# Kernel optimization log

Hardware: AMD Instinct MI355X
Metric: run time of the kernel (lower is better)

Reference implementation:

```python
import jax, jax.numpy as jnp
import numpy as np

L, S, N, E, H = 1024, 1024, 8, 1024, 16

def setup_inputs() -> dict:
    key = jax.random.key(0)
    k0, k1, k2, k3 = jax.random.split(key, 4)
    query = jax.random.normal(k0, (L, N, E), jnp.float32)
    key_t = jax.random.normal(k1, (S, N, E), jnp.float32)
    in_proj_weight = jax.random.normal(k2, (3 * E, E), jnp.float32) * (1.0 / np.sqrt(E))
    in_proj_bias = jnp.zeros((3 * E,), jnp.float32)
    attn_bias = jax.random.normal(k3, (N * H, L, S), jnp.float32) * 0.02
    return {"query": query, "key": key_t, "in_proj_weight": in_proj_weight,
            "in_proj_bias": in_proj_bias, "attn_bias": attn_bias}

def reference(query, key, in_proj_weight, in_proj_bias, attn_bias):
    tgt_len, bsz, embed_dim = query.shape
    head_dim = embed_dim // H
    scaling = float(head_dim) ** -0.5  # scale_factor = 1
    # q/k projections: first two embed_dim-row slices of in_proj_weight
    q = query @ in_proj_weight[:embed_dim].T + in_proj_bias[:embed_dim]
    k = key @ in_proj_weight[embed_dim:2 * embed_dim].T + in_proj_bias[embed_dim:2 * embed_dim]
    q = q * scaling
    # (L, N, E) -> (N*H, L, hd)
    q = q.reshape(tgt_len, bsz * H, head_dim).transpose(1, 0, 2)
    k = k.reshape(-1, bsz * H, head_dim).transpose(1, 0, 2)
    # scores: (N*H, L, S), additive bias, then stable softmax
    scores = jnp.einsum('bld,bsd->bls', q, k) + attn_bias
    attn_output_weights = jax.nn.softmax(scores, axis=-1)
    return attn_output_weights
```

## Files before the change

kernel.cpp:

```cpp
#include <hip/hip_runtime.h>
#include <hip/hip_bf16.h>
#include <stdint.h>

#define L_DIM 1024
#define S_DIM 1024
#define N_DIM 8
#define E_DIM 1024
#define H_DIM 16
#define HD    64
#define BH    (N_DIM*H_DIM)
#define M_ROWS (L_DIM*N_DIM)

#define AS1 __attribute__((address_space(1)))
#define AS3 __attribute__((address_space(3)))

typedef __bf16 bf16x8 __attribute__((ext_vector_type(8)));
typedef float  f32x4  __attribute__((ext_vector_type(4)));
typedef _Float16 f16;
typedef _Float16 f16x8 __attribute__((ext_vector_type(8)));
typedef unsigned short u16;
typedef unsigned short u16x8 __attribute__((ext_vector_type(8)));

__device__ inline u16 f2bf(float x){
  unsigned int u = __float_as_uint(x);
  u = (u + 0x7FFFu + ((u >> 16) & 1u)) >> 16;
  return (u16)u;
}

__global__ __launch_bounds__(256) void convert_kernel(
    const float* __restrict__ query, const float* __restrict__ key,
    const float* __restrict__ w,
    u16* __restrict__ qbf, u16* __restrict__ kbf,
    u16* __restrict__ wq, u16* __restrict__ wk)
{
  const int QN = M_ROWS*E_DIM;
  const int WN = E_DIM*E_DIM;
  const int total8 = (2*QN + 2*WN)/8;
  int stride = gridDim.x*blockDim.x;
  for (int g = blockIdx.x*blockDim.x + threadIdx.x; g < total8; g += stride) {
    int base = g*8;
    const float* src; u16* dst; float scale = 1.0f;
    if (base < QN)           { src = query + base;      dst = qbf + base; }
    else if (base < 2*QN)    { src = key + (base-QN);   dst = kbf + (base-QN); }
    else if (base < 2*QN+WN) { src = w + (base-2*QN);   dst = wq + (base-2*QN); scale = 0.125f; }
    else                     { src = w + (base-2*QN);   dst = wk + (base-2*QN-WN); }
    float4 v0 = *(const float4*)(src);
    float4 v1 = *(const float4*)(src+4);
    u16x8 o;
    o[0]=f2bf(v0.x*scale); o[1]=f2bf(v0.y*scale); o[2]=f2bf(v0.z*scale); o[3]=f2bf(v0.w*scale);
    o[4]=f2bf(v1.x*scale); o[5]=f2bf(v1.y*scale); o[6]=f2bf(v1.z*scale); o[7]=f2bf(v1.w*scale);
    *(u16x8*)dst = o;
  }
}

__global__ __launch_bounds__(256) void proj_gemm(
    const u16* __restrict__ A, const u16* __restrict__ W,
    const float* __restrict__ bias, float bscale,
    u16* __restrict__ C)
{
  __shared__ __align__(16) u16 As[128*32];
  __shared__ __align__(16) u16 Bs[128*32];
  const int t = threadIdx.x;
  const int lane = t & 63;
  const int w = t >> 6;
  const int wr = w >> 1, wc = w & 1;
  const int rowTile = blockIdx.x * 128;
  const int colTile = blockIdx.y * 128;

  f32x4 acc[4][4];
  #pragma unroll
  for (int m=0;m<4;m++)
    #pragma unroll
    for (int n=0;n<4;n++) acc[m][n] = (f32x4){0.f,0.f,0.f,0.f};

  uint32_t asBase = (uint32_t)(uintptr_t)&As[0];
  uint32_t bsBase = (uint32_t)(uintptr_t)&Bs[0];
  const char* Ab = (const char*)A;
  const char* Wb = (const char*)W;

  for (int kt = 0; kt < 32; ++kt) {
    __syncthreads();
    #pragma unroll
    for (int issue = 0; issue < 2; ++issue) {
      int o = issue*4096 + t*16;
      int row  = o >> 6;
      int colb = o & 63;
      const char* ga = Ab + (size_t)(rowTile + row)*2048 + kt*64 + colb;
      const char* gb = Wb + (size_t)(colTile + row)*2048 + kt*64 + colb;
      uint32_t la = asBase + issue*4096 + (w<<10);
      uint32_t lb = bsBase + issue*4096 + (w<<10);
      __builtin_amdgcn_global_load_lds(
          (const AS1 void*)(uintptr_t)ga, (AS3 void*)(uintptr_t)la, 16, 0, 0);
      __builtin_amdgcn_global_load_lds(
          (const AS1 void*)(uintptr_t)gb, (AS3 void*)(uintptr_t)lb, 16, 0, 0);
    }
    __syncthreads();

    bf16x8 af[4], bfr[4];
    int krow = (lane >> 4) * 16;
    #pragma unroll
    for (int m=0;m<4;m++) {
      int r = wr*64 + m*16 + (lane&15);
      af[m] = *(const bf16x8*)((const char*)As + r*64 + krow);
    }
    #pragma unroll
    for (int n=0;n<4;n++) {
      int r = wc*64 + n*16 + (lane&15);
      bfr[n] = *(const bf16x8*)((const char*)Bs + r*64 + krow);
    }
    #pragma unroll
    for (int m=0;m<4;m++)
      #pragma unroll
      for (int n=0;n<4;n++)
        acc[m][n] = __builtin_amdgcn_mfma_f32_16x16x32_bf16(af[m], bfr[n], acc[m][n], 0,0,0);
  }

  #pragma unroll
  for (int n2=0;n2<4;n2++) {
    int gcol = colTile + wc*64 + n2*16 + (lane&15);
    int h = gcol >> 6, d = gcol & 63;
    float bv = bias[gcol]*bscale;
    #pragma unroll
    for (int m=0;m<4;m++) {
      int grow0 = rowTile + wr*64 + m*16 + ((lane>>4)<<2);
      #pragma unroll
      for (int r=0;r<4;r++) {
        int grow = grow0 + r;
        int l = grow >> 3, nn = grow & 7;
        C[((size_t)(nn*16 + h)*1024 + l)*64 + d] = f2bf(acc[m][n2][r] + bv);
      }
    }
  }
}

__global__ __launch_bounds__(256) void attn_softmax(
    const u16* __restrict__ Qh, const u16* __restrict__ Kh,
    const float* __restrict__ bias, float* __restrict__ out)
{
  __shared__ __align__(16) char scb[16*2048];
  __shared__ __align__(16) char kbuf[8192];
  const int t = threadIdx.x;
  const int lane = t & 63;
  const int w = t >> 6;
  const int ltile = blockIdx.x;
  const int b = blockIdx.y;

  const char* Kb = (const char*)(Kh + (size_t)b*1024*64);
  const u16*  Qb = Qh + (size_t)b*1024*64 + (size_t)ltile*16*64;

  int qoff = (lane&15)*64 + (lane>>4)*8;
  bf16x8 a0 = *(const bf16x8*)(Qb + qoff);
  bf16x8 a1 = *(const bf16x8*)(Qb + qoff + 32);

  const int rowBase = (lane>>4)*4;
  uint32_t kbase = (uint32_t)(uintptr_t)&kbuf[0];

  for (int g = 0; g < 16; ++g) {
    __syncthreads();
    #pragma unroll
    for (int rd = 0; rd < 2; ++rd) {
      int o = rd*4096 + t*16;
      int src = o ^ (((o>>7)&7)<<4);
      __builtin_amdgcn_global_load_lds(
          (const AS1 void*)(uintptr_t)(Kb + (size_t)g*8192 + src),
          (AS3 void*)(uintptr_t)(kbase + rd*4096 + (w<<10)), 16, 0, 0);
    }
    __syncthreads();

    int r = w*16 + (lane&15);
    int byte0 = r*128 + ((lane>>4)*16);
    int swzk = (r&7)<<4;
    bf16x8 b0 = *(const bf16x8*)(kbuf + ((byte0      ) ^ swzk));
    bf16x8 b1 = *(const bf16x8*)(kbuf + ((byte0 + 64 ) ^ swzk));
    f32x4 acc = {0.f,0.f,0.f,0.f};
    acc = __builtin_amdgcn_mfma_f32_16x16x32_bf16(a0, b0, acc, 0,0,0);
    acc = __builtin_amdgcn_mfma_f32_16x16x32_bf16(a1, b1, acc, 0,0,0);

    int scol = g*64 + w*16 + (lane & 15);
    #pragma unroll
    for (int rr=0;rr<4;rr++) {
      int row = rowBase + rr;
      int byte = (row*2048 + scol*2) ^ ((row&7)<<4);
      *(f16*)(scb + byte) = (f16)acc[rr];
    }
  }
  __syncthreads();

  #pragma unroll
  for (int rr=0;rr<4;rr++) {
    int row = rr*4 + w;
    int l_glob = ltile*16 + row;
    const float* brow = bias + ((size_t)b*1024 + l_glob)*1024;
    float*       orow = out  + ((size_t)b*1024 + l_glob)*1024;
    const int swz = (row&7)<<4;
    float v[16];
    float mx = -1e30f;
    #pragma unroll
    for (int it=0; it<2; ++it) {
      int cb = it*1024 + lane*16;
      f16x8 s8 = *(const f16x8*)(scb + ((row*2048 + cb) ^ swz));
      int col = it*512 + lane*8;
      f32x4 b4a = *(const f32x4*)(brow + col);
      f32x4 b4b = *(const f32x4*)(brow + col + 4);
      #pragma unroll
      for (int j=0;j<4;j++) v[it*8+j]   = (float)s8[j]   + b4a[j];
      #pragma unroll
      for (int j=0;j<4;j++) v[it*8+4+j] = (float)s8[4+j] + b4b[j];
    }
    #pragma unroll
    for (int j=0;j<16;j++) mx = fmaxf(mx, v[j]);
    #pragma unroll
    for (int off=32; off>0; off>>=1) mx = fmaxf(mx, __shfl_xor(mx, off, 64));
    float sum = 0.f;
    #pragma unroll
    for (int j=0;j<16;j++) { v[j] = __expf(v[j]-mx); sum += v[j]; }
    #pragma unroll
    for (int off=32; off>0; off>>=1) sum += __shfl_xor(sum, off, 64);
    float inv = 1.0f / sum;
    #pragma unroll
    for (int it=0; it<2; ++it) {
      int col = it*512 + lane*8;
      f32x4 o4a = { v[it*8+0]*inv, v[it*8+1]*inv, v[it*8+2]*inv, v[it*8+3]*inv };
      f32x4 o4b = { v[it*8+4]*inv, v[it*8+5]*inv, v[it*8+6]*inv, v[it*8+7]*inv };
      *(f32x4*)(orow + col)     = o4a;
      *(f32x4*)(orow + col + 4) = o4b;
    }
  }
}

extern "C" void kernel_launch(void* const* d_in, const int* in_sizes, int n_in,
                              void* d_out, int out_size, void* d_ws, size_t ws_size,
                              hipStream_t stream) {
  const float* query = (const float*)d_in[0];
  const float* key   = (const float*)d_in[1];
  const float* w     = (const float*)d_in[2];
  const float* bias  = (const float*)d_in[3];
  const float* abias = (const float*)d_in[4];
  float* out = (float*)d_out;

  char* ws = (char*)d_ws;
  const size_t QKB = (size_t)M_ROWS*E_DIM*2;
  const size_t WB  = (size_t)E_DIM*E_DIM*2;
  u16* qbf = (u16*)ws;  ws += QKB;
  u16* kbf = (u16*)ws;  ws += QKB;
  u16* wq  = (u16*)ws;  ws += WB;
  u16* wk  = (u16*)ws;  ws += WB;
  u16* Qh  = (u16*)ws;  ws += QKB;
  u16* Kh  = (u16*)ws;  ws += QKB;

  hipLaunchKernelGGL(convert_kernel, dim3(2048), dim3(256), 0, stream,
                     query, key, w, qbf, kbf, wq, wk);
  hipLaunchKernelGGL(proj_gemm, dim3(64, 8), dim3(256), 0, stream,
                     qbf, wq, bias, 0.125f, Qh);
  hipLaunchKernelGGL(proj_gemm, dim3(64, 8), dim3(256), 0, stream,
                     kbf, wk, bias + 1024, 1.0f, Kh);
  hipLaunchKernelGGL(attn_softmax, dim3(64, 128), dim3(256), 0, stream,
                     Qh, Kh, abias, out);
}
```

Measured before the change: 322.3 us.

## Compute transposed scores in registers with bias-initialized accumulators, drop LDS staging

The attention-softmax kernel now computes K·Q^T with MFMA so each lane holds four consecutive score columns for one query row. The accumulators are initialized straight from the attention bias, and the fp16 LDS score buffer and the K staging through LDS are removed. Row max and sum are reduced with shuffles plus a small LDS cross-wave exchange. This removes the shared-memory round trip and the per-K-chunk barriers, and it keeps scores in fp32 instead of fp16. In exchange it uses more registers (64 accumulators per lane) and reads K directly from global memory in each wave.

After: 419.0 us. +30.0%, slower.

```diff
diff --git a/kernel.cpp b/kernel.cpp
--- a/kernel.cpp
+++ b/kernel.cpp
@@ -16,8 +16,6 @@
 
 typedef __bf16 bf16x8 __attribute__((ext_vector_type(8)));
 typedef float  f32x4  __attribute__((ext_vector_type(4)));
-typedef _Float16 f16;
-typedef _Float16 f16x8 __attribute__((ext_vector_type(8)));
 typedef unsigned short u16;
 typedef unsigned short u16x8 __attribute__((ext_vector_type(8)));
 
@@ -137,94 +135,73 @@
     const u16* __restrict__ Qh, const u16* __restrict__ Kh,
     const float* __restrict__ bias, float* __restrict__ out)
 {
-  __shared__ __align__(16) char scb[16*2048];
-  __shared__ __align__(16) char kbuf[8192];
+  __shared__ float red_max[4][16];
+  __shared__ float red_sum[4][16];
   const int t = threadIdx.x;
   const int lane = t & 63;
   const int w = t >> 6;
   const int ltile = blockIdx.x;
   const int b = blockIdx.y;
-
-  const char* Kb = (const char*)(Kh + (size_t)b*1024*64);
-  const u16*  Qb = Qh + (size_t)b*1024*64 + (size_t)ltile*16*64;
-
-  int qoff = (lane&15)*64 + (lane>>4)*8;
-  bf16x8 a0 = *(const bf16x8*)(Qb + qoff);
-  bf16x8 a1 = *(const bf16x8*)(Qb + qoff + 32);
-
-  const int rowBase = (lane>>4)*4;
-  uint32_t kbase = (uint32_t)(uintptr_t)&kbuf[0];
-
-  for (int g = 0; g < 16; ++g) {
-    __syncthreads();
-    #pragma unroll
-    for (int rd = 0; rd < 2; ++rd) {
-      int o = rd*4096 + t*16;
-      int src = o ^ (((o>>7)&7)<<4);
-      __builtin_amdgcn_global_load_lds(
-          (const AS1 void*)(uintptr_t)(Kb + (size_t)g*8192 + src),
-          (AS3 void*)(uintptr_t)(kbase + rd*4096 + (w<<10)), 16, 0, 0);
-    }
-    __syncthreads();
-
-    int r = w*16 + (lane&15);
-    int byte0 = r*128 + ((lane>>4)*16);
-    int swzk = (r&7)<<4;
-    bf16x8 b0 = *(const bf16x8*)(kbuf + ((byte0      ) ^ swzk));
-    bf16x8 b1 = *(const bf16x8*)(kbuf + ((byte0 + 64 ) ^ swzk));
-    f32x4 acc = {0.f,0.f,0.f,0.f};
-    acc = __builtin_amdgcn_mfma_f32_16x16x32_bf16(a0, b0, acc, 0,0,0);
-    acc = __builtin_amdgcn_mfma_f32_16x16x32_bf16(a1, b1, acc, 0,0,0);
-
-    int scol = g*64 + w*16 + (lane & 15);
-    #pragma unroll
-    for (int rr=0;rr<4;rr++) {
-      int row = rowBase + rr;
-      int byte = (row*2048 + scol*2) ^ ((row&7)<<4);
-      *(f16*)(scb + byte) = (f16)acc[rr];
-    }
-  }
+  const int q  = lane & 15;
+  const int sg = lane >> 4;
+
+  const u16* Qb = Qh + (size_t)b*65536 + (size_t)ltile*16*64;
+  bf16x8 a0 = *(const bf16x8*)(Qb + q*64 + sg*8);
+  bf16x8 a1 = *(const bf16x8*)(Qb + q*64 + sg*8 + 32);
+
+  const u16* Kw = Kh + (size_t)b*65536 + (size_t)w*16384 + (lane&15)*64 + sg*8;
+
+  const size_t rowoff = (((size_t)b<<10) + (size_t)ltile*16 + q)*1024 + w*256 + sg*4;
+  const float* bp = bias + rowoff;
+  float*       op = out  + rowoff;
+
+  f32x4 acc[16];
+  #pragma unroll
+  for (int st = 0; st < 16; ++st)
+    acc[st] = *(const f32x4*)(bp + st*16);
+
+  #pragma unroll
+  for (int st = 0; st < 16; ++st) {
+    const u16* kp = Kw + st*1024;
+    bf16x8 k0 = *(const bf16x8*)kp;
+    bf16x8 k1 = *(const bf16x8*)(kp + 32);
+    acc[st] = __builtin_amdgcn_mfma_f32_16x16x32_bf16(k0, a0, acc[st], 0,0,0);
+    acc[st] = __builtin_amdgcn_mfma_f32_16x16x32_bf16(k1, a1, acc[st], 0,0,0);
+  }
+
+  float mx = fmaxf(fmaxf(acc[0][0], acc[0][1]), fmaxf(acc[0][2], acc[0][3]));
+  #pragma unroll
+  for (int st = 1; st < 16; ++st) {
+    mx = fmaxf(mx, fmaxf(fmaxf(acc[st][0], acc[st][1]),
+                         fmaxf(acc[st][2], acc[st][3])));
+  }
+  mx = fmaxf(mx, __shfl_xor(mx, 16, 64));
+  mx = fmaxf(mx, __shfl_xor(mx, 32, 64));
+  if (lane < 16) red_max[w][lane] = mx;
   __syncthreads();
-
-  #pragma unroll
-  for (int rr=0;rr<4;rr++) {
-    int row = rr*4 + w;
-    int l_glob = ltile*16 + row;
-    const float* brow = bias + ((size_t)b*1024 + l_glob)*1024;
-    float*       orow = out  + ((size_t)b*1024 + l_glob)*1024;
-    const int swz = (row&7)<<4;
-    float v[16];
-    float mx = -1e30f;
-    #pragma unroll
-    for (int it=0; it<2; ++it) {
-      int cb = it*1024 + lane*16;
-      f16x8 s8 = *(const f16x8*)(scb + ((row*2048 + cb) ^ swz));
-      int col = it*512 + lane*8;
-      f32x4 b4a = *(const f32x4*)(brow + col);
-      f32x4 b4b = *(const f32x4*)(brow + col + 4);
-      #pragma unroll
-      for (int j=0;j<4;j++) v[it*8+j]   = (float)s8[j]   + b4a[j];
-      #pragma unroll
-      for (int j=0;j<4;j++) v[it*8+4+j] = (float)s8[4+j] + b4b[j];
-    }
-    #pragma unroll
-    for (int j=0;j<16;j++) mx = fmaxf(mx, v[j]);
-    #pragma unroll
-    for (int off=32; off>0; off>>=1) mx = fmaxf(mx, __shfl_xor(mx, off, 64));
-    float sum = 0.f;
-    #pragma unroll
-    for (int j=0;j<16;j++) { v[j] = __expf(v[j]-mx); sum += v[j]; }
-    #pragma unroll
-    for (int off=32; off>0; off>>=1) sum += __shfl_xor(sum, off, 64);
-    float inv = 1.0f / sum;
-    #pragma unroll
-    for (int it=0; it<2; ++it) {
-      int col = it*512 + lane*8;
-      f32x4 o4a = { v[it*8+0]*inv, v[it*8+1]*inv, v[it*8+2]*inv, v[it*8+3]*inv };
-      f32x4 o4b = { v[it*8+4]*inv, v[it*8+5]*inv, v[it*8+6]*inv, v[it*8+7]*inv };
-      *(f32x4*)(orow + col)     = o4a;
-      *(f32x4*)(orow + col + 4) = o4b;
-    }
+  mx = fmaxf(fmaxf(red_max[0][q], red_max[1][q]),
+             fmaxf(red_max[2][q], red_max[3][q]));
+
+  float sum = 0.f;
+  #pragma unroll
+  for (int st = 0; st < 16; ++st) {
+    #pragma unroll
+    for (int r = 0; r < 4; ++r) {
+      float e = __expf(acc[st][r] - mx);
+      acc[st][r] = e;
+      sum += e;
+    }
+  }
+  sum += __shfl_xor(sum, 16, 64);
+  sum += __shfl_xor(sum, 32, 64);
+  if (lane < 16) red_sum[w][lane] = sum;
+  __syncthreads();
+  float inv = 1.0f / (red_sum[0][q] + red_sum[1][q] + red_sum[2][q] + red_sum[3][q]);
+
+  #pragma unroll
+  for (int st = 0; st < 16; ++st) {
+    f32x4 o4 = { acc[st][0]*inv, acc[st][1]*inv, acc[st][2]*inv, acc[st][3]*inv };
+    *(f32x4*)(op + st*16) = o4;
   }
 }
 
```

## Fuse fp32-to-bf16 activation conversion into projection GEMM tile loads

Applied to the files above, without the earlier changes.

Removes the separate conversion pass for query and key: the projection GEMM now loads fp32 activation tiles directly into LDS with an XOR swizzle and converts to bf16 while building MFMA fragments. Only the weights are still pre-converted by a smaller kernel. This removes a large intermediate write and read round trip, at the cost of doubled A-tile LDS footprint, wider global loads per tile, and conversion work inside the inner loop.

Result: slower. 335.6 us (+4.1%).

```diff
diff --git a/kernel.cpp b/kernel.cpp
--- a/kernel.cpp
+++ b/kernel.cpp
@@ -16,6 +16,7 @@
 
 typedef __bf16 bf16x8 __attribute__((ext_vector_type(8)));
 typedef float  f32x4  __attribute__((ext_vector_type(4)));
+typedef float  f32x8  __attribute__((ext_vector_type(8)));
 typedef _Float16 f16;
 typedef _Float16 f16x8 __attribute__((ext_vector_type(8)));
 typedef unsigned short u16;
@@ -27,45 +28,39 @@
   return (u16)u;
 }
 
-__global__ __launch_bounds__(256) void convert_kernel(
-    const float* __restrict__ query, const float* __restrict__ key,
+__global__ __launch_bounds__(256) void convert_w(
     const float* __restrict__ w,
-    u16* __restrict__ qbf, u16* __restrict__ kbf,
     u16* __restrict__ wq, u16* __restrict__ wk)
 {
-  const int QN = M_ROWS*E_DIM;
   const int WN = E_DIM*E_DIM;
-  const int total8 = (2*QN + 2*WN)/8;
-  int stride = gridDim.x*blockDim.x;
-  for (int g = blockIdx.x*blockDim.x + threadIdx.x; g < total8; g += stride) {
-    int base = g*8;
-    const float* src; u16* dst; float scale = 1.0f;
-    if (base < QN)           { src = query + base;      dst = qbf + base; }
-    else if (base < 2*QN)    { src = key + (base-QN);   dst = kbf + (base-QN); }
-    else if (base < 2*QN+WN) { src = w + (base-2*QN);   dst = wq + (base-2*QN); scale = 0.125f; }
-    else                     { src = w + (base-2*QN);   dst = wk + (base-2*QN-WN); }
-    float4 v0 = *(const float4*)(src);
-    float4 v1 = *(const float4*)(src+4);
-    u16x8 o;
-    o[0]=f2bf(v0.x*scale); o[1]=f2bf(v0.y*scale); o[2]=f2bf(v0.z*scale); o[3]=f2bf(v0.w*scale);
-    o[4]=f2bf(v1.x*scale); o[5]=f2bf(v1.y*scale); o[6]=f2bf(v1.z*scale); o[7]=f2bf(v1.w*scale);
-    *(u16x8*)dst = o;
-  }
+  int g = blockIdx.x*blockDim.x + threadIdx.x;
+  int base = g*8;
+  const float* src; u16* dst; float scale;
+  if (base < WN) { src = w + base; dst = wq + base;      scale = 0.125f; }
+  else           { src = w + base; dst = wk + (base-WN); scale = 1.0f;   }
+  float4 v0 = *(const float4*)(src);
+  float4 v1 = *(const float4*)(src+4);
+  u16x8 o;
+  o[0]=f2bf(v0.x*scale); o[1]=f2bf(v0.y*scale); o[2]=f2bf(v0.z*scale); o[3]=f2bf(v0.w*scale);
+  o[4]=f2bf(v1.x*scale); o[5]=f2bf(v1.y*scale); o[6]=f2bf(v1.z*scale); o[7]=f2bf(v1.w*scale);
+  *(u16x8*)dst = o;
 }
 
 __global__ __launch_bounds__(256) void proj_gemm(
-    const u16* __restrict__ A, const u16* __restrict__ W,
+    const float* __restrict__ A, const u16* __restrict__ W,
     const float* __restrict__ bias, float bscale,
     u16* __restrict__ C)
 {
-  __shared__ __align__(16) u16 As[128*32];
-  __shared__ __align__(16) u16 Bs[128*32];
+  __shared__ __align__(16) float Asf[128*32];
+  __shared__ __align__(16) u16  Bs[128*32];
   const int t = threadIdx.x;
   const int lane = t & 63;
   const int w = t >> 6;
   const int wr = w >> 1, wc = w & 1;
   const int rowTile = blockIdx.x * 128;
   const int colTile = blockIdx.y * 128;
+  const int q16 = lane & 15;
+  const int sg  = lane >> 4;
 
   f32x4 acc[4][4];
   #pragma unroll
@@ -73,40 +68,51 @@
     #pragma unroll
     for (int n=0;n<4;n++) acc[m][n] = (f32x4){0.f,0.f,0.f,0.f};
 
-  uint32_t asBase = (uint32_t)(uintptr_t)&As[0];
+  uint32_t asBase = (uint32_t)(uintptr_t)&Asf[0];
   uint32_t bsBase = (uint32_t)(uintptr_t)&Bs[0];
   const char* Ab = (const char*)A;
   const char* Wb = (const char*)W;
 
   for (int kt = 0; kt < 32; ++kt) {
     __syncthreads();
+    #pragma unroll
+    for (int issue = 0; issue < 4; ++issue) {
+      int o = issue*4096 + t*16;
+      int row  = o >> 7;
+      int colb = o & 127;
+      int scol = colb ^ ((row&7)<<4);
+      const char* ga = Ab + (size_t)(rowTile + row)*4096 + kt*128 + scol;
+      uint32_t la = asBase + issue*4096 + (w<<10);
+      __builtin_amdgcn_global_load_lds(
+          (const AS1 void*)(uintptr_t)ga, (AS3 void*)(uintptr_t)la, 16, 0, 0);
+    }
     #pragma unroll
     for (int issue = 0; issue < 2; ++issue) {
       int o = issue*4096 + t*16;
       int row  = o >> 6;
       int colb = o & 63;
-      const char* ga = Ab + (size_t)(rowTile + row)*2048 + kt*64 + colb;
       const char* gb = Wb + (size_t)(colTile + row)*2048 + kt*64 + colb;
-      uint32_t la = asBase + issue*4096 + (w<<10);
       uint32_t lb = bsBase + issue*4096 + (w<<10);
       __builtin_amdgcn_global_load_lds(
-          (const AS1 void*)(uintptr_t)ga, (AS3 void*)(uintptr_t)la, 16, 0, 0);
-      __builtin_amdgcn_global_load_lds(
           (const AS1 void*)(uintptr_t)gb, (AS3 void*)(uintptr_t)lb, 16, 0, 0);
     }
     __syncthreads();
 
     bf16x8 af[4], bfr[4];
-    int krow = (lane >> 4) * 16;
     #pragma unroll
     for (int m=0;m<4;m++) {
-      int r = wr*64 + m*16 + (lane&15);
-      af[m] = *(const bf16x8*)((const char*)As + r*64 + krow);
+      int r = wr*64 + m*16 + q16;
+      int swk = (r&7)<<4;
+      const char* rb = (const char*)Asf + r*128;
+      f32x4 lo = *(const f32x4*)(rb + ((sg*32   ) ^ swk));
+      f32x4 hi = *(const f32x4*)(rb + ((sg*32+16) ^ swk));
+      f32x8 a8 = __builtin_shufflevector(lo, hi, 0,1,2,3,4,5,6,7);
+      af[m] = __builtin_convertvector(a8, bf16x8);
     }
     #pragma unroll
     for (int n=0;n<4;n++) {
-      int r = wc*64 + n*16 + (lane&15);
-      bfr[n] = *(const bf16x8*)((const char*)Bs + r*64 + krow);
+      int r = wc*64 + n*16 + q16;
+      bfr[n] = *(const bf16x8*)((const char*)Bs + r*64 + sg*16);
     }
     #pragma unroll
     for (int m=0;m<4;m++)
@@ -117,12 +123,12 @@
 
   #pragma unroll
   for (int n2=0;n2<4;n2++) {
-    int gcol = colTile + wc*64 + n2*16 + (lane&15);
+    int gcol = colTile + wc*64 + n2*16 + q16;
     int h = gcol >> 6, d = gcol & 63;
     float bv = bias[gcol]*bscale;
     #pragma unroll
     for (int m=0;m<4;m++) {
-      int grow0 = rowTile + wr*64 + m*16 + ((lane>>4)<<2);
+      int grow0 = rowTile + wr*64 + m*16 + (sg<<2);
       #pragma unroll
       for (int r=0;r<4;r++) {
         int grow = grow0 + r;
@@ -241,19 +247,17 @@
   char* ws = (char*)d_ws;
   const size_t QKB = (size_t)M_ROWS*E_DIM*2;
   const size_t WB  = (size_t)E_DIM*E_DIM*2;
-  u16* qbf = (u16*)ws;  ws += QKB;
-  u16* kbf = (u16*)ws;  ws += QKB;
   u16* wq  = (u16*)ws;  ws += WB;
   u16* wk  = (u16*)ws;  ws += WB;
   u16* Qh  = (u16*)ws;  ws += QKB;
   u16* Kh  = (u16*)ws;  ws += QKB;
 
-  hipLaunchKernelGGL(convert_kernel, dim3(2048), dim3(256), 0, stream,
-                     query, key, w, qbf, kbf, wq, wk);
+  hipLaunchKernelGGL(convert_w, dim3(2*E_DIM*E_DIM/8/256), dim3(256), 0, stream,
+                     w, wq, wk);
   hipLaunchKernelGGL(proj_gemm, dim3(64, 8), dim3(256), 0, stream,
-                     qbf, wq, bias, 0.125f, Qh);
+                     query, wq, bias, 0.125f, Qh);
   hipLaunchKernelGGL(proj_gemm, dim3(64, 8), dim3(256), 0, stream,
-                     kbf, wk, bias + 1024, 1.0f, Kh);
+                     key, wk, bias + 1024, 1.0f, Kh);
   hipLaunchKernelGGL(attn_softmax, dim3(64, 128), dim3(256), 0, stream,
                      Qh, Kh, abias, out);
 }
```
